# Performance work log

Hardware: AMD Instinct MI355X
Metric: run time of the kernel (lower is better)

Reference implementation:

```python
import jax, jax.numpy as jnp
import numpy as np

D, LEN_IN, LEN_OUT = 2, 1, 10
H1, H2 = 32, 32
B, T = 4096, 512
F_IN = D * LEN_IN          # 2
F_OUT = D * LEN_OUT        # 20


def setup_inputs() -> dict:
    key = jax.random.key(0)
    ks = jax.random.split(key, 12)
    s = 1.0 / np.sqrt(H1)  # PyTorch default init scale for LSTMCell/Linear
    u = lambda k, shape: jax.random.uniform(k, shape, jnp.float32, -s, s)
    return {
        "x": jax.random.normal(ks[0], (B, T, F_IN), jnp.float32),
        # LSTMCell 1 (input 2 -> hidden 32); gate order i,f,g,o stacked on dim 0
        "W_ih1": u(ks[1], (4 * H1, F_IN)),
        "W_hh1": u(ks[2], (4 * H1, H1)),
        "b_ih1": u(ks[3], (4 * H1,)),
        "b_hh1": u(ks[4], (4 * H1,)),
        # LSTMCell 2 (32 -> 32)
        "W_ih2": u(ks[5], (4 * H2, H1)),
        "W_hh2": u(ks[6], (4 * H2, H2)),
        "b_ih2": u(ks[7], (4 * H2,)),
        "b_hh2": u(ks[8], (4 * H2,)),
        # Final linear 32 -> 20
        "W_out": u(ks[9], (F_OUT, H2)),
        "b_out": u(ks[10], (F_OUT,)),
    }


def _lstm_cell(x, h, c, W_ih, W_hh, b):
    # gates: [B, 4H]; PyTorch gate order i, f, g, o
    gates = x @ W_ih.T + h @ W_hh.T + b
    i, f, g, o = jnp.split(gates, 4, axis=-1)
    i, f, o = jax.nn.sigmoid(i), jax.nn.sigmoid(f), jax.nn.sigmoid(o)
    g = jnp.tanh(g)
    c_new = f * c + i * g
    h_new = o * jnp.tanh(c_new)
    return h_new, c_new


def reference(x, W_ih1, W_hh1, b_ih1, b_hh1, W_ih2, W_hh2, b_ih2, b_hh2, W_out, b_out):
    b1 = b_ih1 + b_hh1
    b2 = b_ih2 + b_hh2
    Bsz = x.shape[0]
    h1 = jnp.zeros((Bsz, H1), x.dtype)
    c1 = jnp.zeros((Bsz, H1), x.dtype)
    h2 = jnp.zeros((Bsz, H2), x.dtype)
    c2 = jnp.zeros((Bsz, H2), x.dtype)

    def step(carry, x_t):
        h1, c1, h2, c2 = carry
        h1, c1 = _lstm_cell(x_t, h1, c1, W_ih1, W_hh1, b1)
        h2, c2 = _lstm_cell(h1, h2, c2, W_ih2, W_hh2, b2)
        out_t = h2 @ W_out.T + b_out  # [B, 20]
        return (h1, c1, h2, c2), out_t

    xs = jnp.swapaxes(x, 0, 1)  # [T, B, F_IN]
    _, outs = jax.lax.scan(step, (h1, c1, h2, c2), xs)  # outs: [T, B, 20]
    outs = jnp.swapaxes(outs, 0, 1)  # [B, T, 20]
    return outs.reshape(Bsz, x.shape[1], D, LEN_OUT)
```

## Files before the change

kernel.cpp:

```cpp
#include <hip/hip_runtime.h>
#include <hip/hip_fp16.h>

#define TLEN 512
#define HDIM 32
#define FOUT 20
#define HST  36

typedef __attribute__((ext_vector_type(8))) short bf16x8;
typedef __attribute__((ext_vector_type(4))) float f32x4;
typedef __attribute__((ext_vector_type(4))) short s16x4;

__device__ __forceinline__ float sigm(float v) {
  float e = __builtin_amdgcn_exp2f(-1.4426950408889634f * v);
  return __builtin_amdgcn_rcpf(1.0f + e);
}
__device__ __forceinline__ float tanh_f(float v) {
  float e = __builtin_amdgcn_exp2f(2.8853900817779268f * v);
  return 1.0f - 2.0f * __builtin_amdgcn_rcpf(1.0f + e);
}
__device__ __forceinline__ void hilo(float v, short& h, short& l) {
  unsigned u = __builtin_bit_cast(unsigned, v);
  unsigned r = u + 0x7fffu + ((u >> 16) & 1u);
  h = (short)(r >> 16);
  float hf = __builtin_bit_cast(float, r & 0xffff0000u);
  float res = v - hf;
  unsigned u2 = __builtin_bit_cast(unsigned, res);
  unsigned r2 = u2 + 0x7fffu + ((u2 >> 16) & 1u);
  l = (short)(r2 >> 16);
}

__device__ __forceinline__ void barrier_lgkm() {
  asm volatile("s_waitcnt lgkmcnt(0)\n\ts_barrier" ::: "memory");
}

__device__ __forceinline__ bf16x8 read_h(const short* buf, int off) {
  s16x4 a = *(const s16x4*)(buf + off);
  s16x4 b = *(const s16x4*)(buf + off + 4);
  bf16x8 r;
  r[0]=a[0]; r[1]=a[1]; r[2]=a[2]; r[3]=a[3];
  r[4]=b[0]; r[5]=b[1]; r[6]=b[2]; r[7]=b[3];
  return r;
}

__device__ __forceinline__ float lstm_update(const f32x4& g, float& c) {
  float iv = sigm(g[0]), fv = sigm(g[1]), gv = tanh_f(g[2]), ov = sigm(g[3]);
  c = fv * c + iv * gv;
  return ov * tanh_f(c);
}

__global__ __launch_bounds__(1024, 1) void lstm_seq_kernel(
    const float* __restrict__ xg,
    const float* __restrict__ Wih1, const float* __restrict__ Whh1,
    const float* __restrict__ bih1, const float* __restrict__ bhh1,
    const float* __restrict__ Wih2, const float* __restrict__ Whh2,
    const float* __restrict__ bih2, const float* __restrict__ bhh2,
    const float* __restrict__ Wout, const float* __restrict__ bout,
    float* __restrict__ out)
{
  __shared__ __half xl[16 * 1028];
  __shared__ short h1hiB[2][16 * HST], h1loB[2][16 * HST];
  __shared__ short h2hiB[2][16 * HST], h2loB[2][16 * HST];

  const int tid  = threadIdx.x;
  const int w    = tid >> 6;
  const int lane = tid & 63;
  const int n    = lane & 15;
  const int q    = lane >> 4;
  const int q4   = q * 4;
  const int q8   = q * 8;
  const int b0   = blockIdx.x * 16;
  const bool isL1 = (w < 8);
  const int wr   = w & 7;
  const int p    = w & 1;
  const int pr   = w >> 1;

  for (int idx = tid; idx < 16 * 1024; idx += 1024) {
    int row = idx >> 10, col = idx & 1023;
    xl[row * 1028 + col] = __float2half(xg[((size_t)(b0 + row) << 10) + col]);
  }

  const int og = (n & 3) * HDIM + 4 * wr + (n >> 2);
  bf16x8 WAh, WAl, WBh, WBl;
  float bc[4], wx0[4], wx1[4], boc[4];
  bf16x8 WoH = {0,0,0,0,0,0,0,0}, WoL = {0,0,0,0,0,0,0,0};
  if (isL1) {
    #pragma unroll
    for (int j = 0; j < 8; j++) {
      short hh, ll;
      hilo(Whh1[og * HDIM + q8 + j], hh, ll); WAh[j] = hh; WAl[j] = ll;
    }
    #pragma unroll
    for (int r = 0; r < 4; r++) {
      int gr = r * HDIM + 4 * wr + q;
      bc[r]  = bih1[gr] + bhh1[gr];
      wx0[r] = Wih1[gr * 2 + 0];
      wx1[r] = Wih1[gr * 2 + 1];
      int orow = 16 * p + q4 + r;
      boc[r] = (orow < FOUT) ? bout[orow] : 0.0f;
    }
    int orow = 16 * p + n;
    if (orow < FOUT) {
      #pragma unroll
      for (int j = 0; j < 8; j++) {
        short hh, ll;
        hilo(Wout[orow * HDIM + q8 + j], hh, ll); WoH[j] = hh; WoL[j] = ll;
      }
    }
  } else {
    #pragma unroll
    for (int j = 0; j < 8; j++) {
      short hh, ll;
      hilo(Wih2[og * HDIM + q8 + j], hh, ll); WAh[j] = hh; WAl[j] = ll;
      hilo(Whh2[og * HDIM + q8 + j], hh, ll); WBh[j] = hh; WBl[j] = ll;
    }
    #pragma unroll
    for (int r = 0; r < 4; r++) {
      int gr = r * HDIM + 4 * wr + q;
      bc[r] = bih2[gr] + bhh2[gr];
    }
  }

  const int hoff = n * HST + 4 * wr + q;
  const int aoff = n * HST + q8;
  float c = 0.0f;

  bf16x8 h1h = {0,0,0,0,0,0,0,0}, h1l = {0,0,0,0,0,0,0,0};
  bf16x8 h2h = {0,0,0,0,0,0,0,0}, h2l = {0,0,0,0,0,0,0,0};

  __syncthreads();

  if (isL1) {
    __half2 hv = *(const __half2*)&xl[n * 1028];
    float xv0 = __half2float(hv.x), xv1 = __half2float(hv.y);
    f32x4 g1;
    #pragma unroll
    for (int r = 0; r < 4; r++) g1[r] = fmaf(xv1, wx1[r], fmaf(xv0, wx0[r], bc[r]));
    float h1n = lstm_update(g1, c);
    short hh, ll; hilo(h1n, hh, ll);
    h1hiB[0][hoff] = hh; h1loB[0][hoff] = ll;
  }
  barrier_lgkm();
  h1h = read_h(h1hiB[0], aoff);
  h1l = read_h(h1loB[0], aoff);

#define STEP(T, PAR, DS3, HR3, XV0, XV1)                                          \
  {                                                                               \
    if (isL1) {                                                                   \
      f32x4 g1;                                                                   \
      _Pragma("unroll") for (int r = 0; r < 4; r++)                               \
        g1[r] = fmaf((XV1), wx1[r], fmaf((XV0), wx0[r], bc[r]));                  \
      g1 = __builtin_amdgcn_mfma_f32_16x16x32_bf16(WAh, h1h, g1, 0, 0, 0);        \
      g1 = __builtin_amdgcn_mfma_f32_16x16x32_bf16(WAl, h1h, g1, 0, 0, 0);        \
      g1 = __builtin_amdgcn_mfma_f32_16x16x32_bf16(WAh, h1l, g1, 0, 0, 0);        \
      float h1n = lstm_update(g1, c);                                             \
      short hh, ll; hilo(h1n, hh, ll);                                            \
      h1hiB[PAR][hoff] = hh; h1loB[PAR][hoff] = ll;                               \
    } else {                                                                      \
      f32x4 ga, gb;                                                               \
      _Pragma("unroll") for (int r = 0; r < 4; r++) { ga[r] = bc[r]; gb[r] = 0.0f; } \
      ga = __builtin_amdgcn_mfma_f32_16x16x32_bf16(WAh, h1h, ga, 0, 0, 0);        \
      gb = __builtin_amdgcn_mfma_f32_16x16x32_bf16(WBh, h2h, gb, 0, 0, 0);        \
      ga = __builtin_amdgcn_mfma_f32_16x16x32_bf16(WAl, h1h, ga, 0, 0, 0);        \
      gb = __builtin_amdgcn_mfma_f32_16x16x32_bf16(WBl, h2h, gb, 0, 0, 0);        \
      ga = __builtin_amdgcn_mfma_f32_16x16x32_bf16(WAh, h1l, ga, 0, 0, 0);        \
      gb = __builtin_amdgcn_mfma_f32_16x16x32_bf16(WBh, h2l, gb, 0, 0, 0);        \
      f32x4 g2;                                                                   \
      _Pragma("unroll") for (int r = 0; r < 4; r++) g2[r] = ga[r] + gb[r];        \
      float h2n = lstm_update(g2, c);                                             \
      short hh, ll; hilo(h2n, hh, ll);                                            \
      h2hiB[PAR][hoff] = hh; h2loB[PAR][hoff] = ll;                               \
    }                                                                             \
    barrier_lgkm();                                   \
    h1h = read_h(h1hiB[PAR], aoff);                                               \
    h1l = read_h(h1loB[PAR], aoff);                                               \
                    \
    if ((DS3) >= 0 && isL1 && pr == (DS3)) {                                      \
      f32x4 ao;                                                                   \
      _Pragma("unroll") for (int r = 0; r < 4; r++) ao[r] = boc[r];               \
      ao = __builtin_amdgcn_mfma_f32_16x16x32_bf16(WoH, h2h, ao, 0, 0, 0);        \
      ao = __builtin_amdgcn_mfma_f32_16x16x32_bf16(WoL, h2h, ao, 0, 0, 0);        \
      ao = __builtin_amdgcn_mfma_f32_16x16x32_bf16(WoH, h2l, ao, 0, 0, 0);        \
      if (p == 0 || q == 0) {                                                     \
        float4 st = { ao[0], ao[1], ao[2], ao[3] };                               \
        *(float4*)&out[((size_t)(b0 + n) * TLEN + ((T) - 2)) * FOUT + 16 * p + q4] = st; \
      }                                                                           \
    }                                                                             \
    if (!isL1 || pr == (HR3)) {                                                   \
      h2h = read_h(h2hiB[PAR], aoff);                                             \
      h2l = read_h(h2loB[PAR], aoff);                                             \
    }                                                                             \
  }

  {
    float a0 = 0.f, a1 = 0.f;
    if (isL1) { __half2 hv = *(const __half2*)&xl[n * 1028 + 2]; a0 = __half2float(hv.x); a1 = __half2float(hv.y); }
    STEP(1, 1, -1, 0, a0, a1);
    if (isL1) { __half2 hv = *(const __half2*)&xl[n * 1028 + 4]; a0 = __half2float(hv.x); a1 = __half2float(hv.y); }
    STEP(2, 0, 0, 1, a0, a1);
    if (isL1) { __half2 hv = *(const __half2*)&xl[n * 1028 + 6]; a0 = __half2float(hv.x); a1 = __half2float(hv.y); }
    STEP(3, 1, 1, 2, a0, a1);
  }

  for (int t = 4; t < TLEN; t += 4) {
    float xv[8] = {0.f, 0.f, 0.f, 0.f, 0.f, 0.f, 0.f, 0.f};
    if (isL1) {
      const short* xp = (const short*)xl + n * 1028 + 2 * t;
      s16x4 xa = *(const s16x4*)xp;
      s16x4 xb = *(const s16x4*)(xp + 4);
      #pragma unroll
      for (int j = 0; j < 4; j++) {
        xv[j]     = __half2float(__builtin_bit_cast(__half, (short)xa[j]));
        xv[4 + j] = __half2float(__builtin_bit_cast(__half, (short)xb[j]));
      }
    }
    STEP(t + 0, 0, 2, 3, xv[0], xv[1]);
    STEP(t + 1, 1, 3, 0, xv[2], xv[3]);
    STEP(t + 2, 0, 0, 1, xv[4], xv[5]);
    STEP(t + 3, 1, 1, 2, xv[6], xv[7]);
  }
#undef STEP

  if (!isL1) {
    f32x4 ga, gb;
    #pragma unroll
    for (int r = 0; r < 4; r++) { ga[r] = bc[r]; gb[r] = 0.0f; }
    ga = __builtin_amdgcn_mfma_f32_16x16x32_bf16(WAh, h1h, ga, 0, 0, 0);
    gb = __builtin_amdgcn_mfma_f32_16x16x32_bf16(WBh, h2h, gb, 0, 0, 0);
    ga = __builtin_amdgcn_mfma_f32_16x16x32_bf16(WAl, h1h, ga, 0, 0, 0);
    gb = __builtin_amdgcn_mfma_f32_16x16x32_bf16(WBl, h2h, gb, 0, 0, 0);
    ga = __builtin_amdgcn_mfma_f32_16x16x32_bf16(WAh, h1l, ga, 0, 0, 0);
    gb = __builtin_amdgcn_mfma_f32_16x16x32_bf16(WBh, h2l, gb, 0, 0, 0);
    f32x4 g2;
    #pragma unroll
    for (int r = 0; r < 4; r++) g2[r] = ga[r] + gb[r];
    float h2n = lstm_update(g2, c);
    short hh, ll; hilo(h2n, hh, ll);
    h2hiB[0][hoff] = hh; h2loB[0][hoff] = ll;
  } else if (pr == 2) {
    const int s = TLEN - 2;
    f32x4 ao;
    #pragma unroll
    for (int r = 0; r < 4; r++) ao[r] = boc[r];
    ao = __builtin_amdgcn_mfma_f32_16x16x32_bf16(WoH, h2h, ao, 0, 0, 0);
    ao = __builtin_amdgcn_mfma_f32_16x16x32_bf16(WoL, h2h, ao, 0, 0, 0);
    ao = __builtin_amdgcn_mfma_f32_16x16x32_bf16(WoH, h2l, ao, 0, 0, 0);
    if (p == 0 || q == 0) {
      float4 st = { ao[0], ao[1], ao[2], ao[3] };
      *(float4*)&out[((size_t)(b0 + n) * TLEN + s) * FOUT + 16 * p + q4] = st;
    }
  }
  barrier_lgkm();

  if (isL1 && pr == 3) {
    h2h = read_h(h2hiB[0], aoff);
    h2l = read_h(h2loB[0], aoff);
    const int s = TLEN - 1;
    f32x4 ao;
    #pragma unroll
    for (int r = 0; r < 4; r++) ao[r] = boc[r];
    ao = __builtin_amdgcn_mfma_f32_16x16x32_bf16(WoH, h2h, ao, 0, 0, 0);
    ao = __builtin_amdgcn_mfma_f32_16x16x32_bf16(WoL, h2h, ao, 0, 0, 0);
    ao = __builtin_amdgcn_mfma_f32_16x16x32_bf16(WoH, h2l, ao, 0, 0, 0);
    if (p == 0 || q == 0) {
      float4 st = { ao[0], ao[1], ao[2], ao[3] };
      *(float4*)&out[((size_t)(b0 + n) * TLEN + s) * FOUT + 16 * p + q4] = st;
    }
  }
}

extern "C" void kernel_launch(void* const* d_in, const int* in_sizes, int n_in,
                              void* d_out, int out_size, void* d_ws, size_t ws_size,
                              hipStream_t stream) {
  const float* xg   = (const float*)d_in[0];
  const float* Wih1 = (const float*)d_in[1];
  const float* Whh1 = (const float*)d_in[2];
  const float* bih1 = (const float*)d_in[3];
  const float* bhh1 = (const float*)d_in[4];
  const float* Wih2 = (const float*)d_in[5];
  const float* Whh2 = (const float*)d_in[6];
  const float* bih2 = (const float*)d_in[7];
  const float* bhh2 = (const float*)d_in[8];
  const float* Wout = (const float*)d_in[9];
  const float* bout = (const float*)d_in[10];
  float* out = (float*)d_out;

  hipLaunchKernelGGL(lstm_seq_kernel, dim3(256), dim3(1024), 0, stream,
                     xg, Wih1, Whh1, bih1, bhh1, Wih2, Whh2, bih2, bhh2, Wout, bout, out);
}
```

Baseline: 442.6 us.

## Deepen LSTM layer skew to two steps with four-slot shared hidden buffers

Layer 2 now runs two time steps behind layer 1 instead of one, using a 4-deep ring of shared-memory hidden-state buffers and double-buffered h1 registers on the layer-2 waves. Layer-2 waves read h1 one step ahead so its LDS load latency is hidden behind the following step's compute. The output projection is likewise delayed an extra step, and extra drain steps handle the tail. This costs more LDS, more registers, and more complex prologue and epilogue logic that could hide indexing mistakes.

```diff
diff --git a/kernel.cpp b/kernel.cpp
--- a/kernel.cpp
+++ b/kernel.cpp
@@ -58,8 +58,8 @@
     float* __restrict__ out)
 {
   __shared__ __half xl[16 * 1028];
-  __shared__ short h1hiB[2][16 * HST], h1loB[2][16 * HST];
-  __shared__ short h2hiB[2][16 * HST], h2loB[2][16 * HST];
+  __shared__ short h1hiB[4][16 * HST], h1loB[4][16 * HST];
+  __shared__ short h2hiB[4][16 * HST], h2loB[4][16 * HST];
 
   const int tid  = threadIdx.x;
   const int w    = tid >> 6;
@@ -125,6 +125,7 @@
   float c = 0.0f;
 
   bf16x8 h1h = {0,0,0,0,0,0,0,0}, h1l = {0,0,0,0,0,0,0,0};
+  bf16x8 h1nh = {0,0,0,0,0,0,0,0}, h1nl = {0,0,0,0,0,0,0,0};
   bf16x8 h2h = {0,0,0,0,0,0,0,0}, h2l = {0,0,0,0,0,0,0,0};
 
   __syncthreads();
@@ -143,62 +144,78 @@
   h1h = read_h(h1hiB[0], aoff);
   h1l = read_h(h1loB[0], aoff);
 
-#define STEP(T, PAR, DS3, HR3, XV0, XV1)                                          \
+#define STEP(S0,S1,S2,S3, TOUT, H1X, H1XL, L1C, L2C, L2H1R, L2H2R, PREAD, EMIT, XV0, XV1) \
   {                                                                               \
     if (isL1) {                                                                   \
-      f32x4 g1;                                                                   \
-      _Pragma("unroll") for (int r = 0; r < 4; r++)                               \
-        g1[r] = fmaf((XV1), wx1[r], fmaf((XV0), wx0[r], bc[r]));                  \
-      g1 = __builtin_amdgcn_mfma_f32_16x16x32_bf16(WAh, h1h, g1, 0, 0, 0);        \
-      g1 = __builtin_amdgcn_mfma_f32_16x16x32_bf16(WAl, h1h, g1, 0, 0, 0);        \
-      g1 = __builtin_amdgcn_mfma_f32_16x16x32_bf16(WAh, h1l, g1, 0, 0, 0);        \
-      float h1n = lstm_update(g1, c);                                             \
-      short hh, ll; hilo(h1n, hh, ll);                                            \
-      h1hiB[PAR][hoff] = hh; h1loB[PAR][hoff] = ll;                               \
+      if (L1C) {                                                                  \
+        f32x4 g1;                                                                 \
+        _Pragma("unroll") for (int r = 0; r < 4; r++)                             \
+          g1[r] = fmaf((XV1), wx1[r], fmaf((XV0), wx0[r], bc[r]));                \
+        g1 = __builtin_amdgcn_mfma_f32_16x16x32_bf16(WAh, h1h, g1, 0, 0, 0);      \
+        g1 = __builtin_amdgcn_mfma_f32_16x16x32_bf16(WAl, h1h, g1, 0, 0, 0);      \
+        g1 = __builtin_amdgcn_mfma_f32_16x16x32_bf16(WAh, h1l, g1, 0, 0, 0);      \
+        float h1n = lstm_update(g1, c);                                           \
+        short hh, ll; hilo(h1n, hh, ll);                                          \
+        h1hiB[S0][hoff] = hh; h1loB[S0][hoff] = ll;                               \
+      }                                                                           \
     } else {                                                                      \
-      f32x4 ga, gb;                                                               \
-      _Pragma("unroll") for (int r = 0; r < 4; r++) { ga[r] = bc[r]; gb[r] = 0.0f; } \
-      ga = __builtin_amdgcn_mfma_f32_16x16x32_bf16(WAh, h1h, ga, 0, 0, 0);        \
-      gb = __builtin_amdgcn_mfma_f32_16x16x32_bf16(WBh, h2h, gb, 0, 0, 0);        \
-      ga = __builtin_amdgcn_mfma_f32_16x16x32_bf16(WAl, h1h, ga, 0, 0, 0);        \
-      gb = __builtin_amdgcn_mfma_f32_16x16x32_bf16(WBl, h2h, gb, 0, 0, 0);        \
-      ga = __builtin_amdgcn_mfma_f32_16x16x32_bf16(WAh, h1l, ga, 0, 0, 0);        \
-      gb = __builtin_amdgcn_mfma_f32_16x16x32_bf16(WBh, h2l, gb, 0, 0, 0);        \
-      f32x4 g2;                                                                   \
-      _Pragma("unroll") for (int r = 0; r < 4; r++) g2[r] = ga[r] + gb[r];        \
-      float h2n = lstm_update(g2, c);                                             \
-      short hh, ll; hilo(h2n, hh, ll);                                            \
-      h2hiB[PAR][hoff] = hh; h2loB[PAR][hoff] = ll;                               \
+      if (L2C) {                                                                  \
+        f32x4 ga, gb;                                                             \
+        _Pragma("unroll") for (int r = 0; r < 4; r++) { ga[r] = bc[r]; gb[r] = 0.0f; } \
+        ga = __builtin_amdgcn_mfma_f32_16x16x32_bf16(WAh, H1X, ga, 0, 0, 0);      \
+        gb = __builtin_amdgcn_mfma_f32_16x16x32_bf16(WBh, h2h, gb, 0, 0, 0);      \
+        ga = __builtin_amdgcn_mfma_f32_16x16x32_bf16(WAl, H1X, ga, 0, 0, 0);      \
+        gb = __builtin_amdgcn_mfma_f32_16x16x32_bf16(WBl, h2h, gb, 0, 0, 0);      \
+        ga = __builtin_amdgcn_mfma_f32_16x16x32_bf16(WAh, H1XL, ga, 0, 0, 0);     \
+        gb = __builtin_amdgcn_mfma_f32_16x16x32_bf16(WBh, h2l, gb, 0, 0, 0);      \
+        f32x4 g2;                                                                 \
+        _Pragma("unroll") for (int r = 0; r < 4; r++) g2[r] = ga[r] + gb[r];      \
+        float h2n = lstm_update(g2, c);                                           \
+        short hh, ll; hilo(h2n, hh, ll);                                          \
+        h2hiB[S2][hoff] = hh; h2loB[S2][hoff] = ll;                               \
+      }                                                                           \
     }                                                                             \
-    barrier_lgkm();                                   \
-    h1h = read_h(h1hiB[PAR], aoff);                                               \
-    h1l = read_h(h1loB[PAR], aoff);                                               \
-                    \
-    if ((DS3) >= 0 && isL1 && pr == (DS3)) {                                      \
-      f32x4 ao;                                                                   \
-      _Pragma("unroll") for (int r = 0; r < 4; r++) ao[r] = boc[r];               \
-      ao = __builtin_amdgcn_mfma_f32_16x16x32_bf16(WoH, h2h, ao, 0, 0, 0);        \
-      ao = __builtin_amdgcn_mfma_f32_16x16x32_bf16(WoL, h2h, ao, 0, 0, 0);        \
-      ao = __builtin_amdgcn_mfma_f32_16x16x32_bf16(WoH, h2l, ao, 0, 0, 0);        \
-      if (p == 0 || q == 0) {                                                     \
-        float4 st = { ao[0], ao[1], ao[2], ao[3] };                               \
-        *(float4*)&out[((size_t)(b0 + n) * TLEN + ((T) - 2)) * FOUT + 16 * p + q4] = st; \
-      }                                                                           \
-    }                                                                             \
-    if (!isL1 || pr == (HR3)) {                                                   \
-      h2h = read_h(h2hiB[PAR], aoff);                                             \
-      h2l = read_h(h2loB[PAR], aoff);                                             \
+    barrier_lgkm();                                                               \
+    if (isL1) {                                                                   \
+      if (L1C) {                                                                  \
+        h1h = read_h(h1hiB[S0], aoff);                                            \
+        h1l = read_h(h1loB[S0], aoff);                                            \
+      }                                                                           \
+      if ((PREAD) && pr == (S2)) {                                                \
+        h2h = read_h(h2hiB[S2], aoff);                                            \
+        h2l = read_h(h2loB[S2], aoff);                                            \
+      }                                                                           \
+      if ((EMIT) && pr == (S3)) {                                                 \
+        f32x4 ao;                                                                 \
+        _Pragma("unroll") for (int r = 0; r < 4; r++) ao[r] = boc[r];             \
+        ao = __builtin_amdgcn_mfma_f32_16x16x32_bf16(WoH, h2h, ao, 0, 0, 0);      \
+        ao = __builtin_amdgcn_mfma_f32_16x16x32_bf16(WoL, h2h, ao, 0, 0, 0);      \
+        ao = __builtin_amdgcn_mfma_f32_16x16x32_bf16(WoH, h2l, ao, 0, 0, 0);      \
+        if (p == 0 || q == 0) {                                                   \
+          float4 st = { ao[0], ao[1], ao[2], ao[3] };                             \
+          *(float4*)&out[((size_t)(b0 + n) * TLEN + (TOUT)) * FOUT + 16 * p + q4] = st; \
+        }                                                                         \
+      }                                                                           \
+    } else {                                                                      \
+      if (L2H1R) {                                                                \
+        H1X  = read_h(h1hiB[S0], aoff);                                           \
+        H1XL = read_h(h1loB[S0], aoff);                                           \
+      }                                                                           \
+      if (L2H2R) {                                                                \
+        h2h = read_h(h2hiB[S2], aoff);                                            \
+        h2l = read_h(h2loB[S2], aoff);                                            \
+      }                                                                           \
     }                                                                             \
   }
 
   {
     float a0 = 0.f, a1 = 0.f;
     if (isL1) { __half2 hv = *(const __half2*)&xl[n * 1028 + 2]; a0 = __half2float(hv.x); a1 = __half2float(hv.y); }
-    STEP(1, 1, -1, 0, a0, a1);
+    STEP(1,0,3,2, 0, h1nh,h1nl, 1,0,1,0,0,0, a0, a1);
     if (isL1) { __half2 hv = *(const __half2*)&xl[n * 1028 + 4]; a0 = __half2float(hv.x); a1 = __half2float(hv.y); }
-    STEP(2, 0, 0, 1, a0, a1);
+    STEP(2,1,0,3, 0, h1h,h1l,   1,1,1,1,1,0, a0, a1);
     if (isL1) { __half2 hv = *(const __half2*)&xl[n * 1028 + 6]; a0 = __half2float(hv.x); a1 = __half2float(hv.y); }
-    STEP(3, 1, 1, 2, a0, a1);
+    STEP(3,2,1,0, 0, h1nh,h1nl, 1,1,1,1,1,1, a0, a1);
   }
 
   for (int t = 4; t < TLEN; t += 4) {
@@ -213,47 +230,60 @@
         xv[4 + j] = __half2float(__builtin_bit_cast(__half, (short)xb[j]));
       }
     }
-    STEP(t + 0, 0, 2, 3, xv[0], xv[1]);
-    STEP(t + 1, 1, 3, 0, xv[2], xv[3]);
-    STEP(t + 2, 0, 0, 1, xv[4], xv[5]);
-    STEP(t + 3, 1, 1, 2, xv[6], xv[7]);
+    STEP(0,3,2,1, t - 3, h1h,h1l,   1,1,1,1,1,1, xv[0], xv[1]);
+    STEP(1,0,3,2, t - 2, h1nh,h1nl, 1,1,1,1,1,1, xv[2], xv[3]);
+    STEP(2,1,0,3, t - 1, h1h,h1l,   1,1,1,1,1,1, xv[4], xv[5]);
+    STEP(3,2,1,0, t,     h1nh,h1nl, 1,1,1,1,1,1, xv[6], xv[7]);
   }
 #undef STEP
 
-  if (!isL1) {
-    f32x4 ga, gb;
-    #pragma unroll
-    for (int r = 0; r < 4; r++) { ga[r] = bc[r]; gb[r] = 0.0f; }
-    ga = __builtin_amdgcn_mfma_f32_16x16x32_bf16(WAh, h1h, ga, 0, 0, 0);
-    gb = __builtin_amdgcn_mfma_f32_16x16x32_bf16(WBh, h2h, gb, 0, 0, 0);
-    ga = __builtin_amdgcn_mfma_f32_16x16x32_bf16(WAl, h1h, ga, 0, 0, 0);
-    gb = __builtin_amdgcn_mfma_f32_16x16x32_bf16(WBl, h2h, gb, 0, 0, 0);
-    ga = __builtin_amdgcn_mfma_f32_16x16x32_bf16(WAh, h1l, ga, 0, 0, 0);
-    gb = __builtin_amdgcn_mfma_f32_16x16x32_bf16(WBh, h2l, gb, 0, 0, 0);
-    f32x4 g2;
-    #pragma unroll
-    for (int r = 0; r < 4; r++) g2[r] = ga[r] + gb[r];
-    float h2n = lstm_update(g2, c);
-    short hh, ll; hilo(h2n, hh, ll);
-    h2hiB[0][hoff] = hh; h2loB[0][hoff] = ll;
-  } else if (pr == 2) {
-    const int s = TLEN - 2;
-    f32x4 ao;
-    #pragma unroll
-    for (int r = 0; r < 4; r++) ao[r] = boc[r];
-    ao = __builtin_amdgcn_mfma_f32_16x16x32_bf16(WoH, h2h, ao, 0, 0, 0);
-    ao = __builtin_amdgcn_mfma_f32_16x16x32_bf16(WoL, h2h, ao, 0, 0, 0);
-    ao = __builtin_amdgcn_mfma_f32_16x16x32_bf16(WoH, h2l, ao, 0, 0, 0);
-    if (p == 0 || q == 0) {
-      float4 st = { ao[0], ao[1], ao[2], ao[3] };
-      *(float4*)&out[((size_t)(b0 + n) * TLEN + s) * FOUT + 16 * p + q4] = st;
-    }
-  }
-  barrier_lgkm();
+#define STEP2(S0,S1,S2,S3, TOUT, H1X, H1XL, L2C, L2H2R, PREAD, EMIT)              \
+  {                                                                               \
+    if (!isL1 && (L2C)) {                                                         \
+      f32x4 ga, gb;                                                               \
+      _Pragma("unroll") for (int r = 0; r < 4; r++) { ga[r] = bc[r]; gb[r] = 0.0f; } \
+      ga = __builtin_amdgcn_mfma_f32_16x16x32_bf16(WAh, H1X, ga, 0, 0, 0);        \
+      gb = __builtin_amdgcn_mfma_f32_16x16x32_bf16(WBh, h2h, gb, 0, 0, 0);        \
+      ga = __builtin_amdgcn_mfma_f32_16x16x32_bf16(WAl, H1X, ga, 0, 0, 0);        \
+      gb = __builtin_amdgcn_mfma_f32_16x16x32_bf16(WBl, h2h, gb, 0, 0, 0);        \
+      ga = __builtin_amdgcn_mfma_f32_16x16x32_bf16(WAh, H1XL, ga, 0, 0, 0);       \
+      gb = __builtin_amdgcn_mfma_f32_16x16x32_bf16(WBh, h2l, gb, 0, 0, 0);        \
+      f32x4 g2;                                                                   \
+      _Pragma("unroll") for (int r = 0; r < 4; r++) g2[r] = ga[r] + gb[r];        \
+      float h2n = lstm_update(g2, c);                                             \
+      short hh, ll; hilo(h2n, hh, ll);                                            \
+      h2hiB[S2][hoff] = hh; h2loB[S2][hoff] = ll;                                 \
+    }                                                                             \
+    barrier_lgkm();                                                               \
+    if (isL1) {                                                                   \
+      if ((PREAD) && pr == (S2)) {                                                \
+        h2h = read_h(h2hiB[S2], aoff);                                            \
+        h2l = read_h(h2loB[S2], aoff);                                            \
+      }                                                                           \
+      if ((EMIT) && pr == (S3)) {                                                 \
+        f32x4 ao;                                                                 \
+        _Pragma("unroll") for (int r = 0; r < 4; r++) ao[r] = boc[r];             \
+        ao = __builtin_amdgcn_mfma_f32_16x16x32_bf16(WoH, h2h, ao, 0, 0, 0);      \
+        ao = __builtin_amdgcn_mfma_f32_16x16x32_bf16(WoL, h2h, ao, 0, 0, 0);      \
+        ao = __builtin_amdgcn_mfma_f32_16x16x32_bf16(WoH, h2l, ao, 0, 0, 0);      \
+        if (p == 0 || q == 0) {                                                   \
+          float4 st = { ao[0], ao[1], ao[2], ao[3] };                             \
+          *(float4*)&out[((size_t)(b0 + n) * TLEN + (TOUT)) * FOUT + 16 * p + q4] = st; \
+        }                                                                         \
+      }                                                                           \
+    } else {                                                                      \
+      if (L2H2R) {                                                                \
+        h2h = read_h(h2hiB[S2], aoff);                                            \
+        h2l = read_h(h2loB[S2], aoff);                                            \
+      }                                                                           \
+    }                                                                             \
+  }
+
+  STEP2(0,3,2,1, TLEN - 3, h1h,h1l, 1, 1, 1, 1);
+  STEP2(1,0,3,2, TLEN - 2, h1nh,h1nl, 1, 0, 1, 1);
+#undef STEP2
 
   if (isL1 && pr == 3) {
-    h2h = read_h(h2hiB[0], aoff);
-    h2l = read_h(h2loB[0], aoff);
     const int s = TLEN - 1;
     f32x4 ao;
     #pragma unroll
```

Measured after the change: 461.2 us. 4.2% more time.
